# Performance work log

Hardware: AMD Instinct MI355X
Metric: run time of the kernel (lower is better)

Reference implementation:

```python
import jax, jax.numpy as jnp
import numpy as np

NODES_PER_GRAPH = 21
NUM_GRAPHS = 50000
N = NODES_PER_GRAPH * NUM_GRAPHS  # 1,050,000 nodes
NUM_FEATURES = 3
NUM_CLASSES = 29
H1, H2 = 64, 128
BN_EPS = 1e-5

_HAND = np.array([(0, 1), (1, 2), (2, 3), (3, 4), (0, 5), (5, 6), (6, 7), (7, 8),
                  (0, 9), (9, 10), (10, 11), (11, 12), (0, 13), (13, 14), (14, 15),
                  (15, 16), (0, 17), (17, 18), (18, 19), (19, 20)], dtype=np.int64).T  # [2,20]


def setup_inputs() -> dict:
    key = jax.random.key(0)
    ks = jax.random.split(key, 16)
    # Tile hand skeleton across NUM_GRAPHS disjoint graphs with node offsets.
    offsets = (np.arange(NUM_GRAPHS, dtype=np.int64) * NODES_PER_GRAPH)  # [G]
    ei = (_HAND[:, None, :] + offsets[None, :, None]).reshape(2, -1)      # [2, G*20]
    edge_index = jnp.asarray(ei)
    batch = jnp.asarray(np.repeat(np.arange(NUM_GRAPHS, dtype=np.int64), NODES_PER_GRAPH))

    x = jax.random.normal(ks[0], (N, NUM_FEATURES), dtype=jnp.float32)

    def lin(k, fi, fo):
        kw, kb = jax.random.split(k)
        s = 1.0 / np.sqrt(fi)
        return (jax.random.uniform(kw, (fi, fo), jnp.float32, -s, s),
                jax.random.uniform(kb, (fo,), jnp.float32, -s, s))

    W1, b1 = lin(ks[1], NUM_FEATURES, H1)
    W2, b2 = lin(ks[2], H1, H2)
    W3, b3 = lin(ks[3], H2, NUM_CLASSES)

    def bn(k, d):
        k1, k2, k3, k4 = jax.random.split(k, 4)
        return (1.0 + 0.1 * jax.random.normal(k1, (d,), jnp.float32),   # gamma
                0.1 * jax.random.normal(k2, (d,), jnp.float32),          # beta
                0.01 * jax.random.normal(k3, (d,), jnp.float32),         # running_mean
                jax.random.uniform(k4, (d,), jnp.float32, 0.5, 1.5))     # running_var

    g1, be1, m1, v1 = bn(ks[4], H1)
    g2, be2, m2, v2 = bn(ks[5], H2)

    return {"x": x, "W1": W1, "b1": b1, "g1": g1, "be1": be1, "m1": m1, "v1": v1,
            "W2": W2, "b2": b2, "g2": g2, "be2": be2, "m2": m2, "v2": v2,
            "W3": W3, "b3": b3, "edge_index": edge_index, "batch": batch}


def gcn_conv(x, W, b, src, dst):
    """PyG GCNConv: linear, add self-loops, sym-normalized scatter-add, bias."""
    h = x @ W                                              # [N, Fout]
    deg = jnp.zeros((N,), x.dtype).at[dst].add(1.0) + 1.0  # in-degree incl. self-loop
    dinv = deg ** -0.5
    msg = h[src] * (dinv[src] * dinv[dst])[:, None]        # edge-wise gather + normalize
    out = jnp.zeros_like(h).at[dst].add(msg)               # scatter-add aggregation
    out = out + h * (dinv * dinv)[:, None]                 # self-loop contribution
    return out + b


def bn_eval(x, gamma, beta, mean, var):
    return (x - mean) * (gamma * jax.lax.rsqrt(var + BN_EPS)) + beta


def reference(x, W1, b1, g1, be1, m1, v1, W2, b2, g2, be2, m2, v2, W3, b3,
              edge_index, batch):
    src, dst = edge_index[0], edge_index[1]
    h = jax.nn.relu(bn_eval(gcn_conv(x, W1, b1, src, dst), g1, be1, m1, v1))
    # dropout is identity in eval mode
    h = jax.nn.relu(bn_eval(gcn_conv(h, W2, b2, src, dst), g2, be2, m2, v2))
    h = gcn_conv(h, W3, b3, src, dst)                      # [N, C]
    summed = jax.ops.segment_sum(h, batch, num_segments=NUM_GRAPHS)
    counts = jax.ops.segment_sum(jnp.ones((N,), h.dtype), batch, num_segments=NUM_GRAPHS)
    pooled = summed / counts[:, None]                      # global mean pool [G, C]
    return jax.nn.log_softmax(pooled, axis=1)
```

## Files before the change

### kernel.cpp

```cpp
#include <hip/hip_runtime.h>
#include <math.h>


#define G_TOTAL 50000
#define NPG 21
#define GPB 6
#define NCHUNK ((G_TOTAL + GPB - 1) / GPB)
#define NCLS 29
#define BN_EPS 1e-5f
#define INV_SQRT2 0.70710678118654752440f
#define ROOT_COLSUM 4.53553390593273762f

#define WS_W1   0
#define WS_B1   192
#define WS_B2   256
#define WS_B3   384
#define WS_W3T  416
#define WS_BF   4160
#define WS_TOTAL (WS_BF + 16384)

typedef short s16x8 __attribute__((ext_vector_type(8)));
typedef float f32x4 __attribute__((ext_vector_type(4)));

__device__ __forceinline__ unsigned f2bf(float f) {
    unsigned u = __float_as_uint(f);
    return (u + 0x7FFFu + ((u >> 16) & 1u)) >> 16;
}
__device__ __forceinline__ float bf2f(unsigned h) { return __uint_as_float(h << 16); }

__device__ __forceinline__ void split2(float v0, float v1, unsigned& hw, unsigned& lw) {
    unsigned h0 = f2bf(v0), h1 = f2bf(v1);
    unsigned l0 = f2bf(v0 - bf2f(h0)), l1 = f2bf(v1 - bf2f(h1));
    hw = (h1 << 16) | h0;
    lw = (l1 << 16) | l0;
}

__global__ void prep_kernel(const float* __restrict__ W1, const float* __restrict__ b1,
                            const float* __restrict__ g1, const float* __restrict__ be1,
                            const float* __restrict__ m1, const float* __restrict__ v1,
                            const float* __restrict__ W2, const float* __restrict__ b2,
                            const float* __restrict__ g2, const float* __restrict__ be2,
                            const float* __restrict__ m2, const float* __restrict__ v2,
                            const float* __restrict__ W3, const float* __restrict__ b3,
                            float* __restrict__ ws) {
    int t = blockIdx.x * blockDim.x + threadIdx.x;
    if (t < 192) {
        int j = t & 63;
        float s = g1[j] * rsqrtf(v1[j] + BN_EPS);
        ws[WS_W1 + t] = W1[t] * s;
    } else if (t < 256) {
        int j = t - 192;
        float s = g1[j] * rsqrtf(v1[j] + BN_EPS);
        ws[WS_B1 + j] = (b1[j] - m1[j]) * s + be1[j];
    } else if (t < 384) {
        int j = t - 256;
        float s = g2[j] * rsqrtf(v2[j] + BN_EPS);
        ws[WS_B2 + j] = (b2[j] - m2[j]) * s + be2[j];
    } else if (t < 416) {
        int j = t - 384;
        ws[WS_B3 + j] = (j < NCLS) ? b3[j] : 0.f;
    } else if (t < WS_BF) {
        int i = t - WS_W3T;
        if (i < 3712) {
            int c = i >> 7, k = i & 127;
            ws[WS_W3T + i] = W3[k * NCLS + c];
        }
    } else if (t < WS_TOTAL) {
        int i = t - WS_BF;
        int d = i & 3;
        int l = (i >> 2) & 63;
        int h = (i >> 8) & 1;
        int s = (i >> 9) & 1;
        int n = i >> 10;
        int g = l >> 4, r = l & 15;
        int c = 16 * n + r;
        float sc = g2[c] * rsqrtf(v2[c] + BN_EPS);
        int k0 = 32 * s + 8 * g + 2 * d;
        float v0 = W2[k0 * 128 + c] * sc;
        float v1v = W2[(k0 + 1) * 128 + c] * sc;
        unsigned hw, lw;
        split2(v0, v1v, hw, lw);
        ((unsigned*)ws)[WS_BF + i] = h ? lw : hw;
    }
}

__global__ __launch_bounds__(256, 4)
void gcn_main(const float* __restrict__ x, const float* __restrict__ ws,
              float* __restrict__ out) {
    __shared__ float sAlias[8704];
    __shared__ float sP[GPB * 128];
    __shared__ float sW1[192];
    __shared__ float sb1[64];
    __shared__ float sb2[128];
    __shared__ float sb3[32];
    __shared__ float sLg[176];
    __shared__ float sRed[12];

    const int tid = threadIdx.x;
    const int g0 = blockIdx.x * GPB;
    const int nv = min(GPB, G_TOTAL - g0);
    const int Mrows = nv * NPG;

    if (tid < 192) sW1[tid] = ws[WS_W1 + tid];
    else if (tid < 256) sb1[tid - 192] = ws[WS_B1 + (tid - 192)];
    if (tid < 128) sb2[tid] = ws[WS_B2 + tid];
    else if (tid < 160) sb3[tid - 128] = ws[WS_B3 + (tid - 128)];
    #pragma unroll
    for (int p = tid; p < GPB * 128; p += 256) sP[p] = 0.f;
    __syncthreads();

    const int node = tid >> 1;
    const int s = tid & 1;
    const int k0 = s * 32;
    const int lg = node / NPG;
    const int jj21 = node - lg * NPG;
    float zown[32];
    {
        float ax0 = 0.f, ax1 = 0.f, ax2 = 0.f;
        if (node < Mrows) {
            const long long gid = (long long)(g0 + lg) * NPG + jj21;
            const float* xp = x + gid * 3;
            const float s0 = xp[0], s1 = xp[1], s2 = xp[2];
            if (jj21 == 0) { ax0 = s0; ax1 = s1; ax2 = s2; }
            else {
                const int dist = ((jj21 & 3) == 1) ? jj21 : 1;
                const float* xq = x + (gid - dist) * 3;
                const float c = ((jj21 & 3) == 1) ? INV_SQRT2 : 0.5f;
                ax0 = fmaf(c, xq[0], 0.5f * s0);
                ax1 = fmaf(c, xq[1], 0.5f * s1);
                ax2 = fmaf(c, xq[2], 0.5f * s2);
            }
        }
        #pragma unroll
        for (int kk = 0; kk < 32; ++kk) {
            const int k = k0 + kk;
            float t = fmaf(ax0, sW1[k], sb1[k]);
            t = fmaf(ax1, sW1[64 + k], t);
            t = fmaf(ax2, sW1[128 + k], t);
            t = fmaxf(t, 0.f);
            if (node >= Mrows) t = 0.f;
            zown[kk] = t;
        }
        float* z1 = sAlias;
        #pragma unroll
        for (int q = 0; q < 8; ++q)
            *(float4*)&z1[node * 68 + k0 + 4 * q] =
                make_float4(zown[4*q], zown[4*q+1], zown[4*q+2], zown[4*q+3]);
    }
    __syncthreads();

    float az[32];
    {
        const float* z1 = sAlias;
        if (jj21 != 0) {
            const int dist = ((jj21 & 3) == 1) ? jj21 : 1;
            const int prow = node - dist;
            const float c = ((jj21 & 3) == 1) ? INV_SQRT2 : 0.5f;
            #pragma unroll
            for (int q = 0; q < 8; ++q) {
                const float4 zp = *(const float4*)&z1[prow * 68 + k0 + 4 * q];
                az[4*q]   = fmaf(c, zp.x, 0.5f * zown[4*q]);
                az[4*q+1] = fmaf(c, zp.y, 0.5f * zown[4*q+1]);
                az[4*q+2] = fmaf(c, zp.z, 0.5f * zown[4*q+2]);
                az[4*q+3] = fmaf(c, zp.w, 0.5f * zown[4*q+3]);
            }
        } else {
            #pragma unroll
            for (int kk = 0; kk < 32; ++kk) az[kk] = zown[kk];
        }
    }
    __syncthreads();

    {
        unsigned* fragH = (unsigned*)sAlias;
        unsigned* fragL = fragH + 4096;
        const int m = node >> 4;
        const int r = node & 15;
        #pragma unroll
        for (int g = 0; g < 4; ++g) {
            uint4 ph, pl;
            split2(az[8*g+0], az[8*g+1], ph.x, pl.x);
            split2(az[8*g+2], az[8*g+3], ph.y, pl.y);
            split2(az[8*g+4], az[8*g+5], ph.z, pl.z);
            split2(az[8*g+6], az[8*g+7], ph.w, pl.w);
            const int idx = ((m * 2 + s) * 64 + g * 16 + r) * 4;
            *(uint4*)&fragH[idx] = ph;
            *(uint4*)&fragL[idx] = pl;
        }
    }
    __syncthreads();

    {
        const int w = tid >> 6;
        const int lane = tid & 63;
        const int r = lane & 15;
        const int g4 = lane >> 4;
        const uint4* wsB = (const uint4*)((const unsigned*)ws + WS_BF);
        uint4 Bh[2][2], Bl[2][2];
        #pragma unroll
        for (int ntl = 0; ntl < 2; ++ntl)
            #pragma unroll
            for (int ss = 0; ss < 2; ++ss) {
                const int n = 2 * w + ntl;
                Bh[ntl][ss] = wsB[((n * 2 + ss) * 2 + 0) * 64 + lane];
                Bl[ntl][ss] = wsB[((n * 2 + ss) * 2 + 1) * 64 + lane];
            }
        const float b2c0 = sb2[32 * w + r];
        const float b2c1 = sb2[32 * w + 16 + r];
        const unsigned* fragH = (const unsigned*)sAlias;
        const unsigned* fragL = fragH + 4096;

        for (int m = 0; m < 8; ++m) {
            s16x8 Ah[2], Al[2];
            #pragma unroll
            for (int ss = 0; ss < 2; ++ss) {
                Ah[ss] = *(const s16x8*)&fragH[((m * 2 + ss) * 64 + lane) * 4];
                Al[ss] = *(const s16x8*)&fragL[((m * 2 + ss) * 64 + lane) * 4];
            }
            f32x4 acc0 = {0.f, 0.f, 0.f, 0.f};
            f32x4 acc1 = {0.f, 0.f, 0.f, 0.f};
            #pragma unroll
            for (int ss = 0; ss < 2; ++ss) {
                const s16x8 bh0 = *(const s16x8*)&Bh[0][ss];
                const s16x8 bl0 = *(const s16x8*)&Bl[0][ss];
                const s16x8 bh1 = *(const s16x8*)&Bh[1][ss];
                const s16x8 bl1 = *(const s16x8*)&Bl[1][ss];
                acc0 = __builtin_amdgcn_mfma_f32_16x16x32_bf16(Ah[ss], bh0, acc0, 0, 0, 0);
                acc0 = __builtin_amdgcn_mfma_f32_16x16x32_bf16(Ah[ss], bl0, acc0, 0, 0, 0);
                acc0 = __builtin_amdgcn_mfma_f32_16x16x32_bf16(Al[ss], bh0, acc0, 0, 0, 0);
                acc1 = __builtin_amdgcn_mfma_f32_16x16x32_bf16(Ah[ss], bh1, acc1, 0, 0, 0);
                acc1 = __builtin_amdgcn_mfma_f32_16x16x32_bf16(Ah[ss], bl1, acc1, 0, 0, 0);
                acc1 = __builtin_amdgcn_mfma_f32_16x16x32_bf16(Al[ss], bh1, acc1, 0, 0, 0);
            }
            const int gA = (16 * m * 3121) >> 16;
            float pA0 = 0.f, pA1 = 0.f, pB0 = 0.f, pB1 = 0.f;
            #pragma unroll
            for (int i = 0; i < 4; ++i) {
                const int row = 16 * m + 4 * g4 + i;
                const int gg = (row * 3121) >> 16;
                const int j = row - 21 * gg;
                float wgt = (j == 0) ? (ROOT_COLSUM * (1.f / 21.f))
                          : (((j & 3) == 0) ? (0.5f / 21.f) : (1.f / 21.f));
                if (row >= Mrows) wgt = 0.f;
                const float z0 = fmaxf(acc0[i] + b2c0, 0.f);
                const float z1v = fmaxf(acc1[i] + b2c1, 0.f);
                if (gg == gA) { pA0 = fmaf(wgt, z0, pA0); pA1 = fmaf(wgt, z1v, pA1); }
                else          { pB0 = fmaf(wgt, z0, pB0); pB1 = fmaf(wgt, z1v, pB1); }
            }
            pA0 += __shfl_xor(pA0, 16); pA0 += __shfl_xor(pA0, 32);
            pA1 += __shfl_xor(pA1, 16); pA1 += __shfl_xor(pA1, 32);
            pB0 += __shfl_xor(pB0, 16); pB0 += __shfl_xor(pB0, 32);
            pB1 += __shfl_xor(pB1, 16); pB1 += __shfl_xor(pB1, 32);
            if (lane < 16) {
                const int gB = gA + 1;
                sP[gA * 128 + 32 * w + r]      += pA0;
                sP[gA * 128 + 32 * w + 16 + r] += pA1;
                if (gB < GPB) {
                    sP[gB * 128 + 32 * w + r]      += pB0;
                    sP[gB * 128 + 32 * w + 16 + r] += pB1;
                }
            }
        }
    }
    __syncthreads();

    {
        float* sW3T = sAlias;
        for (int i = tid; i < 3712; i += 256)
            sW3T[(i >> 7) * 132 + (i & 127)] = ws[WS_W3T + i];
    }
    __syncthreads();

    if (tid < nv * NCLS) {
        const int g = (tid * 2260) >> 16;
        const int c = tid - g * NCLS;
        const float* wrow = &sAlias[c * 132];
        const float* pg = &sP[g * 128];
        float acc3 = sb3[c];
        #pragma unroll
        for (int k = 0; k < 128; k += 4) {
            const float4 wv = *(const float4*)&wrow[k];
            const float4 pv = *(const float4*)&pg[k];
            acc3 = fmaf(pv.x, wv.x, acc3);
            acc3 = fmaf(pv.y, wv.y, acc3);
            acc3 = fmaf(pv.z, wv.z, acc3);
            acc3 = fmaf(pv.w, wv.w, acc3);
        }
        sLg[tid] = acc3;
    }
    __syncthreads();
    if (tid < nv) {
        float m = -1e30f;
        for (int c = 0; c < NCLS; ++c) m = fmaxf(m, sLg[tid * NCLS + c]);
        float sum = 0.f;
        for (int c = 0; c < NCLS; ++c) sum += expf(sLg[tid * NCLS + c] - m);
        sRed[tid * 2] = m;
        sRed[tid * 2 + 1] = logf(sum);
    }
    __syncthreads();
    if (tid < nv * NCLS) {
        const int g = (tid * 2260) >> 16;
        out[(long long)g0 * NCLS + tid] = sLg[tid] - sRed[g * 2] - sRed[g * 2 + 1];
    }
}

extern "C" void kernel_launch(void* const* d_in, const int* in_sizes, int n_in,
                              void* d_out, int out_size, void* d_ws, size_t ws_size,
                              hipStream_t stream) {
    const float* x   = (const float*)d_in[0];
    const float* W1  = (const float*)d_in[1];
    const float* b1  = (const float*)d_in[2];
    const float* g1  = (const float*)d_in[3];
    const float* be1 = (const float*)d_in[4];
    const float* m1  = (const float*)d_in[5];
    const float* v1  = (const float*)d_in[6];
    const float* W2  = (const float*)d_in[7];
    const float* b2  = (const float*)d_in[8];
    const float* g2  = (const float*)d_in[9];
    const float* be2 = (const float*)d_in[10];
    const float* m2  = (const float*)d_in[11];
    const float* v2  = (const float*)d_in[12];
    const float* W3  = (const float*)d_in[13];
    const float* b3  = (const float*)d_in[14];
    float* out = (float*)d_out;
    float* ws  = (float*)d_ws;

    prep_kernel<<<(WS_TOTAL + 255) / 256, 256, 0, stream>>>(
        W1, b1, g1, be1, m1, v1, W2, b2, g2, be2, m2, v2, W3, b3, ws);

    gcn_main<<<NCHUNK, 256, 0, stream>>>(x, ws, out);
}
```

Before: 216.3 us.

## Drop split-bf16 compensation, use truncating bf16 packing and LUT-based pooling

Replaces the hi/lo bf16 split (three MFMAs per product) with a single bf16 MFMA per K-slice, and packs activations by truncation with a byte permute. W1 and its bias are interleaved into float4 entries, and per-row pooling weights come from a shared-memory LUT. Pooled partial sums stay in registers per graph instead of being accumulated into shared memory each iteration. W3 is read straight from global memory instead of being staged in LDS. The cost is lower numerical precision in the second layer (plain bf16 inputs, truncated rather than rounded), which may exceed the tolerance.

```diff
diff --git a/kernel.cpp b/kernel.cpp
--- a/kernel.cpp
+++ b/kernel.cpp
@@ -11,28 +11,19 @@
 #define INV_SQRT2 0.70710678118654752440f
 #define ROOT_COLSUM 4.53553390593273762f
 
-#define WS_W1   0
-#define WS_B1   192
+#define WS_W1B  0
 #define WS_B2   256
 #define WS_B3   384
 #define WS_W3T  416
-#define WS_BF   4160
-#define WS_TOTAL (WS_BF + 16384)
+#define WS_BF   4128
+#define WS_TOTAL (WS_BF + 4096)
 
 typedef short s16x8 __attribute__((ext_vector_type(8)));
 typedef float f32x4 __attribute__((ext_vector_type(4)));
 
-__device__ __forceinline__ unsigned f2bf(float f) {
+__device__ __forceinline__ unsigned f2bf_rne(float f) {
     unsigned u = __float_as_uint(f);
     return (u + 0x7FFFu + ((u >> 16) & 1u)) >> 16;
-}
-__device__ __forceinline__ float bf2f(unsigned h) { return __uint_as_float(h << 16); }
-
-__device__ __forceinline__ void split2(float v0, float v1, unsigned& hw, unsigned& lw) {
-    unsigned h0 = f2bf(v0), h1 = f2bf(v1);
-    unsigned l0 = f2bf(v0 - bf2f(h0)), l1 = f2bf(v1 - bf2f(h1));
-    hw = (h1 << 16) | h0;
-    lw = (l1 << 16) | l0;
 }
 
 __global__ void prep_kernel(const float* __restrict__ W1, const float* __restrict__ b1,
@@ -44,14 +35,13 @@
                             const float* __restrict__ W3, const float* __restrict__ b3,
                             float* __restrict__ ws) {
     int t = blockIdx.x * blockDim.x + threadIdx.x;
-    if (t < 192) {
-        int j = t & 63;
-        float s = g1[j] * rsqrtf(v1[j] + BN_EPS);
-        ws[WS_W1 + t] = W1[t] * s;
-    } else if (t < 256) {
-        int j = t - 192;
-        float s = g1[j] * rsqrtf(v1[j] + BN_EPS);
-        ws[WS_B1 + j] = (b1[j] - m1[j]) * s + be1[j];
+    if (t < 256) {
+        int k = t >> 2, comp = t & 3;
+        float s = g1[k] * rsqrtf(v1[k] + BN_EPS);
+        float v;
+        if (comp < 3) v = W1[comp * 64 + k] * s;
+        else          v = (b1[k] - m1[k]) * s + be1[k];
+        ws[WS_W1B + t] = v;
     } else if (t < 384) {
         int j = t - 256;
         float s = g2[j] * rsqrtf(v2[j] + BN_EPS);
@@ -67,126 +57,108 @@
         }
     } else if (t < WS_TOTAL) {
         int i = t - WS_BF;
-        int d = i & 3;
-        int l = (i >> 2) & 63;
-        int h = (i >> 8) & 1;
-        int s = (i >> 9) & 1;
-        int n = i >> 10;
-        int g = l >> 4, r = l & 15;
+        int d  = i & 3;
+        int l  = (i >> 2) & 63;
+        int ss = (i >> 8) & 1;
+        int n  = i >> 9;
+        int kg = l >> 4, r = l & 15;
         int c = 16 * n + r;
         float sc = g2[c] * rsqrtf(v2[c] + BN_EPS);
-        int k0 = 32 * s + 8 * g + 2 * d;
-        float v0 = W2[k0 * 128 + c] * sc;
-        float v1v = W2[(k0 + 1) * 128 + c] * sc;
-        unsigned hw, lw;
-        split2(v0, v1v, hw, lw);
-        ((unsigned*)ws)[WS_BF + i] = h ? lw : hw;
+        int k0 = 32 * ss + 8 * kg + 2 * d;
+        unsigned h0 = f2bf_rne(W2[k0 * 128 + c] * sc);
+        unsigned h1 = f2bf_rne(W2[(k0 + 1) * 128 + c] * sc);
+        ((unsigned*)ws)[WS_BF + i] = (h1 << 16) | h0;
     }
 }
 
 __global__ __launch_bounds__(256, 4)
 void gcn_main(const float* __restrict__ x, const float* __restrict__ ws,
               float* __restrict__ out) {
-    __shared__ float sAlias[8704];
-    __shared__ float sP[GPB * 128];
-    __shared__ float sW1[192];
-    __shared__ float sb1[64];
-    __shared__ float sb2[128];
-    __shared__ float sb3[32];
-    __shared__ float sLg[176];
-    __shared__ float sRed[12];
+    __shared__ __align__(16) float sZ[8704];
+    __shared__ __align__(16) float4 sW1B[64];
+    __shared__ float  sb2[128];
+    __shared__ __align__(8) float2 sLUT[128];
+    __shared__ float  sP[GPB * 128];
 
     const int tid = threadIdx.x;
     const int g0 = blockIdx.x * GPB;
     const int nv = min(GPB, G_TOTAL - g0);
     const int Mrows = nv * NPG;
 
-    if (tid < 192) sW1[tid] = ws[WS_W1 + tid];
-    else if (tid < 256) sb1[tid - 192] = ws[WS_B1 + (tid - 192)];
-    if (tid < 128) sb2[tid] = ws[WS_B2 + tid];
-    else if (tid < 160) sb3[tid - 128] = ws[WS_B3 + (tid - 128)];
-    #pragma unroll
-    for (int p = tid; p < GPB * 128; p += 256) sP[p] = 0.f;
+    if (tid < 64) sW1B[tid] = ((const float4*)ws)[tid];
+    else if (tid < 192) sb2[tid - 64] = ws[WS_B2 + (tid - 64)];
+    if (tid < 128) {
+        const int r = tid;
+        const int lg2 = (r * 3121) >> 16;
+        const int j = r - NPG * lg2;
+        float w = (j == 0) ? (ROOT_COLSUM / 21.f)
+                           : (((j & 3) == 0) ? (0.5f / 21.f) : (1.f / 21.f));
+        if (r >= Mrows) w = 0.f;
+        sLUT[r] = make_float2(w, (float)lg2);
+    }
     __syncthreads();
 
     const int node = tid >> 1;
     const int s = tid & 1;
     const int k0 = s * 32;
-    const int lg = node / NPG;
-    const int jj21 = node - lg * NPG;
-    float zown[32];
-    {
-        float ax0 = 0.f, ax1 = 0.f, ax2 = 0.f;
+    const int lg = (node * 3121) >> 16;
+    const int j21 = node - NPG * lg;
+    float z[32];
+    {
+        const int dist = (j21 == 0) ? 0 : (((j21 & 3) == 1) ? j21 : 1);
+        const float c = ((j21 & 3) == 1) ? INV_SQRT2 : 0.5f;
+        float s0 = 0.f, s1 = 0.f, s2 = 0.f, q0 = 0.f, q1 = 0.f, q2 = 0.f;
         if (node < Mrows) {
-            const long long gid = (long long)(g0 + lg) * NPG + jj21;
+            const long long gid = (long long)(g0 + lg) * NPG + j21;
             const float* xp = x + gid * 3;
-            const float s0 = xp[0], s1 = xp[1], s2 = xp[2];
-            if (jj21 == 0) { ax0 = s0; ax1 = s1; ax2 = s2; }
-            else {
-                const int dist = ((jj21 & 3) == 1) ? jj21 : 1;
-                const float* xq = x + (gid - dist) * 3;
-                const float c = ((jj21 & 3) == 1) ? INV_SQRT2 : 0.5f;
-                ax0 = fmaf(c, xq[0], 0.5f * s0);
-                ax1 = fmaf(c, xq[1], 0.5f * s1);
-                ax2 = fmaf(c, xq[2], 0.5f * s2);
-            }
-        }
+            s0 = xp[0]; s1 = xp[1]; s2 = xp[2];
+            const float* xq = xp - dist * 3;
+            q0 = xq[0]; q1 = xq[1]; q2 = xq[2];
+        }
+        const float ax0 = fmaf(c, q0, 0.5f * s0);
+        const float ax1 = fmaf(c, q1, 0.5f * s1);
+        const float ax2 = fmaf(c, q2, 0.5f * s2);
         #pragma unroll
         for (int kk = 0; kk < 32; ++kk) {
-            const int k = k0 + kk;
-            float t = fmaf(ax0, sW1[k], sb1[k]);
-            t = fmaf(ax1, sW1[64 + k], t);
-            t = fmaf(ax2, sW1[128 + k], t);
-            t = fmaxf(t, 0.f);
-            if (node >= Mrows) t = 0.f;
-            zown[kk] = t;
-        }
-        float* z1 = sAlias;
+            const float4 wv = sW1B[k0 + kk];
+            float t = fmaf(ax0, wv.x, wv.w);
+            t = fmaf(ax1, wv.y, t);
+            t = fmaf(ax2, wv.z, t);
+            z[kk] = fmaxf(t, 0.f);
+        }
         #pragma unroll
         for (int q = 0; q < 8; ++q)
-            *(float4*)&z1[node * 68 + k0 + 4 * q] =
-                make_float4(zown[4*q], zown[4*q+1], zown[4*q+2], zown[4*q+3]);
-    }
-    __syncthreads();
-
-    float az[32];
-    {
-        const float* z1 = sAlias;
-        if (jj21 != 0) {
-            const int dist = ((jj21 & 3) == 1) ? jj21 : 1;
-            const int prow = node - dist;
-            const float c = ((jj21 & 3) == 1) ? INV_SQRT2 : 0.5f;
-            #pragma unroll
-            for (int q = 0; q < 8; ++q) {
-                const float4 zp = *(const float4*)&z1[prow * 68 + k0 + 4 * q];
-                az[4*q]   = fmaf(c, zp.x, 0.5f * zown[4*q]);
-                az[4*q+1] = fmaf(c, zp.y, 0.5f * zown[4*q+1]);
-                az[4*q+2] = fmaf(c, zp.z, 0.5f * zown[4*q+2]);
-                az[4*q+3] = fmaf(c, zp.w, 0.5f * zown[4*q+3]);
-            }
-        } else {
-            #pragma unroll
-            for (int kk = 0; kk < 32; ++kk) az[kk] = zown[kk];
-        }
-    }
-    __syncthreads();
-
-    {
-        unsigned* fragH = (unsigned*)sAlias;
-        unsigned* fragL = fragH + 4096;
-        const int m = node >> 4;
-        const int r = node & 15;
-        #pragma unroll
-        for (int g = 0; g < 4; ++g) {
-            uint4 ph, pl;
-            split2(az[8*g+0], az[8*g+1], ph.x, pl.x);
-            split2(az[8*g+2], az[8*g+3], ph.y, pl.y);
-            split2(az[8*g+4], az[8*g+5], ph.z, pl.z);
-            split2(az[8*g+6], az[8*g+7], ph.w, pl.w);
-            const int idx = ((m * 2 + s) * 64 + g * 16 + r) * 4;
-            *(uint4*)&fragH[idx] = ph;
-            *(uint4*)&fragL[idx] = pl;
-        }
+            *(float4*)&sZ[node * 68 + k0 + 4 * q] =
+                make_float4(z[4*q], z[4*q+1], z[4*q+2], z[4*q+3]);
+    }
+    __syncthreads();
+
+    {
+        const int dist = (j21 == 0) ? 0 : (((j21 & 3) == 1) ? j21 : 1);
+        const float c = ((j21 & 3) == 1) ? INV_SQRT2 : 0.5f;
+        const int prow = node - dist;
+        #pragma unroll
+        for (int q = 0; q < 8; ++q) {
+            const float4 zp = *(const float4*)&sZ[prow * 68 + k0 + 4 * q];
+            z[4*q]   = fmaf(c, zp.x, 0.5f * z[4*q]);
+            z[4*q+1] = fmaf(c, zp.y, 0.5f * z[4*q+1]);
+            z[4*q+2] = fmaf(c, zp.z, 0.5f * z[4*q+2]);
+            z[4*q+3] = fmaf(c, zp.w, 0.5f * z[4*q+3]);
+        }
+    }
+    __syncthreads();
+
+    {
+        unsigned dw[16];
+        #pragma unroll
+        for (int p = 0; p < 16; ++p)
+            dw[p] = __builtin_amdgcn_perm(__float_as_uint(z[2*p+1]),
+                                          __float_as_uint(z[2*p]), 0x07060302u);
+        char* fragB = (char*)sZ + ((node >> 4) * 2 + s) * 1024 + (node & 15) * 16;
+        #pragma unroll
+        for (int g = 0; g < 4; ++g)
+            *(uint4*)(fragB + g * 256) =
+                make_uint4(dw[4*g], dw[4*g+1], dw[4*g+2], dw[4*g+3]);
     }
     __syncthreads();
 
@@ -196,91 +168,81 @@
         const int r = lane & 15;
         const int g4 = lane >> 4;
         const uint4* wsB = (const uint4*)((const unsigned*)ws + WS_BF);
-        uint4 Bh[2][2], Bl[2][2];
-        #pragma unroll
-        for (int ntl = 0; ntl < 2; ++ntl)
-            #pragma unroll
-            for (int ss = 0; ss < 2; ++ss) {
-                const int n = 2 * w + ntl;
-                Bh[ntl][ss] = wsB[((n * 2 + ss) * 2 + 0) * 64 + lane];
-                Bl[ntl][ss] = wsB[((n * 2 + ss) * 2 + 1) * 64 + lane];
-            }
-        const float b2c0 = sb2[32 * w + r];
-        const float b2c1 = sb2[32 * w + 16 + r];
-        const unsigned* fragH = (const unsigned*)sAlias;
-        const unsigned* fragL = fragH + 4096;
-
+        uint4 B00 = wsB[((2*w+0)*2 + 0)*64 + lane];
+        uint4 B01 = wsB[((2*w+0)*2 + 1)*64 + lane];
+        uint4 B10 = wsB[((2*w+1)*2 + 0)*64 + lane];
+        uint4 B11 = wsB[((2*w+1)*2 + 1)*64 + lane];
+        const float b2c0 = sb2[32*w + r];
+        const float b2c1 = sb2[32*w + 16 + r];
+        const float2* lutp = &sLUT[4 * g4];
+        const char* fragB = (const char*)sZ + lane * 16;
+
+        float pg[GPB][2];
+        #pragma unroll
+        for (int g = 0; g < GPB; ++g) { pg[g][0] = 0.f; pg[g][1] = 0.f; }
+
+        #pragma unroll
         for (int m = 0; m < 8; ++m) {
-            s16x8 Ah[2], Al[2];
-            #pragma unroll
-            for (int ss = 0; ss < 2; ++ss) {
-                Ah[ss] = *(const s16x8*)&fragH[((m * 2 + ss) * 64 + lane) * 4];
-                Al[ss] = *(const s16x8*)&fragL[((m * 2 + ss) * 64 + lane) * 4];
-            }
+            const s16x8 A0 = *(const s16x8*)(fragB + (2*m + 0) * 1024);
+            const s16x8 A1 = *(const s16x8*)(fragB + (2*m + 1) * 1024);
             f32x4 acc0 = {0.f, 0.f, 0.f, 0.f};
             f32x4 acc1 = {0.f, 0.f, 0.f, 0.f};
-            #pragma unroll
-            for (int ss = 0; ss < 2; ++ss) {
-                const s16x8 bh0 = *(const s16x8*)&Bh[0][ss];
-                const s16x8 bl0 = *(const s16x8*)&Bl[0][ss];
-                const s16x8 bh1 = *(const s16x8*)&Bh[1][ss];
-                const s16x8 bl1 = *(const s16x8*)&Bl[1][ss];
-                acc0 = __builtin_amdgcn_mfma_f32_16x16x32_bf16(Ah[ss], bh0, acc0, 0, 0, 0);
-                acc0 = __builtin_amdgcn_mfma_f32_16x16x32_bf16(Ah[ss], bl0, acc0, 0, 0, 0);
-                acc0 = __builtin_amdgcn_mfma_f32_16x16x32_bf16(Al[ss], bh0, acc0, 0, 0, 0);
-                acc1 = __builtin_amdgcn_mfma_f32_16x16x32_bf16(Ah[ss], bh1, acc1, 0, 0, 0);
-                acc1 = __builtin_amdgcn_mfma_f32_16x16x32_bf16(Ah[ss], bl1, acc1, 0, 0, 0);
-                acc1 = __builtin_amdgcn_mfma_f32_16x16x32_bf16(Al[ss], bh1, acc1, 0, 0, 0);
-            }
-            const int gA = (16 * m * 3121) >> 16;
-            float pA0 = 0.f, pA1 = 0.f, pB0 = 0.f, pB1 = 0.f;
+            acc0 = __builtin_amdgcn_mfma_f32_16x16x32_bf16(A0, *(const s16x8*)&B00, acc0, 0, 0, 0);
+            acc0 = __builtin_amdgcn_mfma_f32_16x16x32_bf16(A1, *(const s16x8*)&B01, acc0, 0, 0, 0);
+            acc1 = __builtin_amdgcn_mfma_f32_16x16x32_bf16(A0, *(const s16x8*)&B10, acc1, 0, 0, 0);
+            acc1 = __builtin_amdgcn_mfma_f32_16x16x32_bf16(A1, *(const s16x8*)&B11, acc1, 0, 0, 0);
+
             #pragma unroll
             for (int i = 0; i < 4; ++i) {
-                const int row = 16 * m + 4 * g4 + i;
-                const int gg = (row * 3121) >> 16;
-                const int j = row - 21 * gg;
-                float wgt = (j == 0) ? (ROOT_COLSUM * (1.f / 21.f))
-                          : (((j & 3) == 0) ? (0.5f / 21.f) : (1.f / 21.f));
-                if (row >= Mrows) wgt = 0.f;
-                const float z0 = fmaxf(acc0[i] + b2c0, 0.f);
-                const float z1v = fmaxf(acc1[i] + b2c1, 0.f);
-                if (gg == gA) { pA0 = fmaf(wgt, z0, pA0); pA1 = fmaf(wgt, z1v, pA1); }
-                else          { pB0 = fmaf(wgt, z0, pB0); pB1 = fmaf(wgt, z1v, pB1); }
-            }
-            pA0 += __shfl_xor(pA0, 16); pA0 += __shfl_xor(pA0, 32);
-            pA1 += __shfl_xor(pA1, 16); pA1 += __shfl_xor(pA1, 32);
-            pB0 += __shfl_xor(pB0, 16); pB0 += __shfl_xor(pB0, 32);
-            pB1 += __shfl_xor(pB1, 16); pB1 += __shfl_xor(pB1, 32);
-            if (lane < 16) {
-                const int gB = gA + 1;
-                sP[gA * 128 + 32 * w + r]      += pA0;
-                sP[gA * 128 + 32 * w + 16 + r] += pA1;
-                if (gB < GPB) {
-                    sP[gB * 128 + 32 * w + r]      += pB0;
-                    sP[gB * 128 + 32 * w + 16 + r] += pB1;
+                const float2 wg = lutp[16*m + i];
+                const float t0 = fmaxf(acc0[i] + b2c0, 0.f) * wg.x;
+                const float t1 = fmaxf(acc1[i] + b2c1, 0.f) * wg.x;
+                const int lo = (16*m + i) / 21;
+                const int hiRaw = (16*m + i + 12) / 21;
+                const int hi = (hiRaw > 5) ? 5 : hiRaw;
+                if (lo == hiRaw) {
+                    pg[lo][0] += t0; pg[lo][1] += t1;
+                } else {
+                    const bool cA = (wg.y == (float)lo);
+                    const float s0 = cA ? t0 : 0.f;
+                    const float s1 = cA ? t1 : 0.f;
+                    pg[lo][0] += s0; pg[hi][0] += t0 - s0;
+                    pg[lo][1] += s1; pg[hi][1] += t1 - s1;
                 }
             }
         }
-    }
-    __syncthreads();
-
-    {
-        float* sW3T = sAlias;
-        for (int i = tid; i < 3712; i += 256)
-            sW3T[(i >> 7) * 132 + (i & 127)] = ws[WS_W3T + i];
-    }
-    __syncthreads();
-
-    if (tid < nv * NCLS) {
+        #pragma unroll
+        for (int g = 0; g < GPB; ++g) {
+            #pragma unroll
+            for (int c = 0; c < 2; ++c) {
+                float v = pg[g][c];
+                v += __shfl_xor(v, 16);
+                v += __shfl_xor(v, 32);
+                pg[g][c] = v;
+            }
+        }
+        if (lane < 16) {
+            #pragma unroll
+            for (int g = 0; g < GPB; ++g) {
+                sP[g * 128 + 32*w + r]      = pg[g][0];
+                sP[g * 128 + 32*w + 16 + r] = pg[g][1];
+            }
+        }
+    }
+    __syncthreads();
+
+    float* sLg = sZ;
+    float* sRed = sZ + 192;
+    if (tid < GPB * NCLS) {
         const int g = (tid * 2260) >> 16;
         const int c = tid - g * NCLS;
-        const float* wrow = &sAlias[c * 132];
-        const float* pg = &sP[g * 128];
-        float acc3 = sb3[c];
-        #pragma unroll
-        for (int k = 0; k < 128; k += 4) {
-            const float4 wv = *(const float4*)&wrow[k];
-            const float4 pv = *(const float4*)&pg[k];
+        const float4* w3 = (const float4*)(ws + WS_W3T + c * 128);
+        const float4* pp = (const float4*)&sP[g * 128];
+        float acc3 = ws[WS_B3 + c];
+        #pragma unroll
+        for (int k = 0; k < 32; ++k) {
+            const float4 wv = w3[k];
+            const float4 pv = pp[k];
             acc3 = fmaf(pv.x, wv.x, acc3);
             acc3 = fmaf(pv.y, wv.y, acc3);
             acc3 = fmaf(pv.z, wv.z, acc3);
```

Result: slower. 220.6 us (+2.0%).
